# Optimization experiments

Measured on AMD Instinct MI355X. Metric: run time of the kernel, lower is better.

Reference implementation:

```python
import jax, jax.numpy as jnp
import numpy as np

D_MODEL = 1024
D_STATE = 16
DT_RANK = 64  # d_model // 16 ('auto')
DT_MIN = 0.001
DT_MAX = 0.1


def setup_inputs() -> dict:
    key = jax.random.key(0)
    ks = jax.random.split(key, 7)
    B, S = 2, 2048
    return {
        "x": jax.random.normal(ks[0], (B, S, D_MODEL), jnp.float32),
        "w_in": jax.random.normal(ks[1], (D_MODEL, D_MODEL), jnp.float32) / np.sqrt(D_MODEL).astype(np.float32),
        "w_x": jax.random.normal(ks[2], (D_MODEL, DT_RANK + 2 * D_STATE), jnp.float32) / np.sqrt(D_MODEL).astype(np.float32),
        "w_dt": jax.random.normal(ks[3], (DT_RANK, D_MODEL), jnp.float32) / np.sqrt(DT_RANK).astype(np.float32),
        "b_dt": jnp.zeros((D_MODEL,), jnp.float32),
        "A_log": jax.random.normal(ks[5], (D_MODEL, D_STATE), jnp.float32) * 0.5,
        "Dp": jax.random.normal(ks[6], (D_MODEL,), jnp.float32),
    }


def reference(x, w_in, w_x, w_dt, b_dt, A_log, Dp):
    # x: (b, s, d)
    x_in = jnp.einsum('bsd,de->bse', x, w_in)          # in_proj, (b,s,d_inner=d)
    proj = jnp.einsum('bsd,dp->bsp', x_in, w_x)        # x_proj, (b,s,dt_rank+2n)
    dt_low, Bm, Cm = jnp.split(proj, [DT_RANK, DT_RANK + D_STATE], axis=-1)
    # dt_proj + softplus + range scaling -> (b,s,d)
    dt = jax.nn.softplus(jnp.einsum('bsr,rd->bsd', dt_low, w_dt) + b_dt) * (DT_MAX - DT_MIN) + DT_MIN
    A = -jnp.exp(A_log)                                # (d, n), strictly negative

    b, s, d = x.shape
    h0 = jnp.zeros((b, d, D_STATE), x.dtype)

    # time-major streams for scan
    dt_tm = jnp.swapaxes(dt, 0, 1)     # (s,b,d)
    u_tm = jnp.swapaxes(x_in, 0, 1)    # (s,b,d)
    B_tm = jnp.swapaxes(Bm, 0, 1)      # (s,b,n)
    C_tm = jnp.swapaxes(Cm, 0, 1)      # (s,b,n)

    def step(h, inp):
        dtt, ut, bt, ct = inp
        dA = dtt[:, :, None] * A                      # (b,d,n) = dt[b,d]*A[d,n]
        barA = jnp.exp(dA)
        # bar_B = dA; source sums the input term over channel dim d (keepdim)
        inp_term = jnp.einsum('bdn,bn,bd->bn', dA, bt, ut)  # (b,n)
        h = barA * h + inp_term[:, None, :]           # broadcast over d
        y = jnp.einsum('bdn,bn->bd', h, ct) + Dp * ut # (b,d)
        return h, y

    _, ys = jax.lax.scan(step, h0, (dt_tm, u_tm, B_tm, C_tm))  # ys: (s,b,d)
    return jnp.swapaxes(ys, 0, 1)                     # (b,s,d)
```

## Files before the change

kernel.cpp:

```cpp
#include <hip/hip_runtime.h>
#include <hip/hip_bf16.h>

#define D_MODEL 1024
#define D_STATE 16
#define DT_RANK 64
#define SEQ 2048
#define BATCH 2
#define M_TOTAL 4096
#define CHUNKS 64
#define CLEN 32
#define LOG2E 1.44269504088896f

typedef __bf16 bf16x8 __attribute__((ext_vector_type(8)));
typedef float f32x4 __attribute__((ext_vector_type(4)));

__device__ __forceinline__ unsigned short f2bf(float f) {
    union { float f; unsigned int u; } v; v.f = f;
    unsigned int r = v.u + 0x7FFFu + ((v.u >> 16) & 1u);
    return (unsigned short)(r >> 16);
}
__device__ __forceinline__ float bf2f(unsigned short u) {
    union { unsigned int i; float f; } v; v.i = ((unsigned int)u) << 16; return v.f;
}
__device__ __forceinline__ void gload16(const void* g, void* l) {
    __builtin_amdgcn_global_load_lds(
        (const __attribute__((address_space(1))) unsigned int*)g,
        (__attribute__((address_space(3))) unsigned int*)l, 16, 0, 0);
}
__device__ __forceinline__ float fexp2(float x) { return __builtin_amdgcn_exp2f(x); }

__global__ void __launch_bounds__(256) k_setup(const float* __restrict__ x,
                                               const float* __restrict__ win,
                                               const float* __restrict__ wx,
                                               const float* __restrict__ alog,
                                               unsigned short* __restrict__ xb,
                                               unsigned short* __restrict__ wib,
                                               unsigned short* __restrict__ bt,
                                               unsigned short* __restrict__ wxT,
                                               unsigned short* __restrict__ wxBC,
                                               float* __restrict__ aneg,
                                               unsigned short* __restrict__ anegT) {
    __shared__ float tile[32][33];
    int blk = blockIdx.x;
    int t = threadIdx.x;
    if (blk < 4096) {
        int i = blk * 256 + t;
        float4 v = reinterpret_cast<const float4*>(x)[i];
        ushort4 o;
        o.x = f2bf(v.x); o.y = f2bf(v.y); o.z = f2bf(v.z); o.w = f2bf(v.w);
        reinterpret_cast<ushort4*>(xb)[i] = o;
    } else if (blk < 5120) {
        int i = (blk - 4096) * 256 + t;
        float4 v = reinterpret_cast<const float4*>(win)[i];
        ushort4 o;
        o.x = f2bf(v.x); o.y = f2bf(v.y); o.z = f2bf(v.z); o.w = f2bf(v.w);
        reinterpret_cast<ushort4*>(wib)[i] = o;
    } else if (blk < 6144) {
        int blk2 = blk - 5120;
        int bx = blk2 & 31, by = blk2 >> 5;
        int tx = t & 31, ty = t >> 5;
        int xc = bx * 32 + tx;
#pragma unroll
        for (int j = 0; j < 4; j++)
            tile[ty + 8 * j][tx] = win[(by * 32 + ty + 8 * j) * D_MODEL + xc];
        __syncthreads();
        int x2 = by * 32 + tx;
#pragma unroll
        for (int j = 0; j < 4; j++)
            bt[(bx * 32 + ty + 8 * j) * D_MODEL + x2] = f2bf(tile[tx][ty + 8 * j]);
    } else if (blk < 6400) {
        int idx = (blk - 6144) * 256 + t;
        int e = idx & 1023, p = idx >> 10;
        wxT[p * D_MODEL + e] = f2bf(wx[e * 96 + p]);
    } else if (blk < 6528) {
        int idx = (blk - 6400) * 256 + t;
        int e = idx & 1023, p = idx >> 10;
        wxBC[p * D_MODEL + e] = f2bf(wx[e * 96 + 64 + p]);
    } else {
        int i = (blk - 6528) * 256 + t;
        float v = -expf(alog[i]);
        aneg[i] = v * LOG2E;
        anegT[(i & 15) * D_MODEL + (i >> 4)] = f2bf(v);
    }
}

__global__ void __launch_bounds__(256) k_prepgemm(const unsigned short* __restrict__ wxT,
                                                  const unsigned short* __restrict__ wib,
                                                  float* __restrict__ Cp) {
    __shared__ unsigned short sA[2][64 * 32];
    __shared__ unsigned short sB[2][128 * 32];
    int bid = blockIdx.x;
    int n0 = (bid & 7) * 128;
    int ks = bid >> 3;
    int kbase = ks * 128;
    int t = threadIdx.x;
    int lane = t & 63;
    int w = t >> 6;
    int c = lane & 15, q = lane >> 4;

    const unsigned short* ga = wxT + (t >> 2) * D_MODEL + (t & 3) * 8 + kbase;
    const unsigned short* gb = wib + (n0 + (t >> 2)) * D_MODEL + (t & 3) * 8 + kbase;

    f32x4 acc[4][2] = {};
    {
        char* la = (char*)&sA[0][0] + w * 1024;
        char* lb = (char*)&sB[0][0] + w * 1024;
        gload16(ga, la);
        gload16(gb, lb);
        gload16(gb + 64 * D_MODEL, lb + 4096);
    }
    int cur = 0;
    for (int it = 0; it < 4; it++) {
        __syncthreads();
        if (it + 1 < 4) {
            int kn = (it + 1) * 32;
            char* la = (char*)&sA[cur ^ 1][0] + w * 1024;
            char* lb = (char*)&sB[cur ^ 1][0] + w * 1024;
            gload16(ga + kn, la);
            gload16(gb + kn, lb);
            gload16(gb + 64 * D_MODEL + kn, lb + 4096);
        }
        bf16x8 af[4], bfr[2];
#pragma unroll
        for (int i = 0; i < 4; i++)
            af[i] = *reinterpret_cast<const bf16x8*>(&sA[cur][(i * 16 + c) * 32 + q * 8]);
#pragma unroll
        for (int j = 0; j < 2; j++)
            bfr[j] = *reinterpret_cast<const bf16x8*>(&sB[cur][(w * 32 + j * 16 + c) * 32 + q * 8]);
#pragma unroll
        for (int i = 0; i < 4; i++)
#pragma unroll
            for (int j = 0; j < 2; j++)
                acc[i][j] = __builtin_amdgcn_mfma_f32_16x16x32_bf16(bfr[j], af[i], acc[i][j], 0, 0, 0);
        cur ^= 1;
    }
#pragma unroll
    for (int i = 0; i < 4; i++) {
        int p = ks * 64 + i * 16 + c;
#pragma unroll
        for (int j = 0; j < 2; j++) {
            int d = n0 + w * 32 + j * 16 + q * 4;
            *reinterpret_cast<f32x4*>(&Cp[p * D_MODEL + d]) = acc[i][j];
        }
    }
}

__global__ void __launch_bounds__(256) k_prepreduce(const float* __restrict__ Cp,
                                                    float* __restrict__ Tt) {
    int idx = blockIdx.x * 256 + threadIdx.x;
    float s = 0.f;
#pragma unroll
    for (int ks = 0; ks < 8; ks++) s += Cp[ks * 65536 + idx];
    Tt[idx] = s;
}

__global__ void __launch_bounds__(256) k_prep2(const float* __restrict__ wdt,
                                               const float* __restrict__ Tt,
                                               unsigned short* __restrict__ bt) {
    __shared__ float sw[DT_RANK][8];
    int m0 = blockIdx.x * 8;
    int tid = threadIdx.x;
    for (int s = tid; s < DT_RANK * 8; s += 256) {
        int r = s >> 3, rr = s & 7;
        sw[r][rr] = wdt[r * D_MODEL + m0 + rr];
    }
    __syncthreads();
    float acc[8][4] = {};
    for (int r = 0; r < DT_RANK; r++) {
        float tv0 = Tt[r * D_MODEL + tid];
        float tv1 = Tt[r * D_MODEL + tid + 256];
        float tv2 = Tt[r * D_MODEL + tid + 512];
        float tv3 = Tt[r * D_MODEL + tid + 768];
#pragma unroll
        for (int rr = 0; rr < 8; rr++) {
            float wv = sw[r][rr];
            acc[rr][0] = fmaf(wv, tv0, acc[rr][0]);
            acc[rr][1] = fmaf(wv, tv1, acc[rr][1]);
            acc[rr][2] = fmaf(wv, tv2, acc[rr][2]);
            acc[rr][3] = fmaf(wv, tv3, acc[rr][3]);
        }
    }
#pragma unroll
    for (int rr = 0; rr < 8; rr++)
#pragma unroll
        for (int i = 0; i < 4; i++)
            bt[(D_MODEL + m0 + rr) * D_MODEL + tid + i * 256] = f2bf(acc[rr][i]);
}

__global__ void __launch_bounds__(256) k_gemm_big(const unsigned short* __restrict__ xb,
                                                  const unsigned short* __restrict__ bt,
                                                  const float* __restrict__ bdt,
                                                  unsigned short* __restrict__ xinb,
                                                  unsigned short* __restrict__ dtb) {
    __shared__ unsigned short sA[2][128 * 64];
    __shared__ unsigned short sB[2][128 * 64];
    int bid = blockIdx.x;
    int m0 = (bid & 31) * 128;
    int nt = bid >> 5;
    int n0 = nt * 128;
    int t = threadIdx.x;
    int lane = t & 63;
    int w = t >> 6;
    int wm = (w >> 1) * 64, wn = (w & 1) * 64;
    int c = lane & 15, q = lane >> 4;

    const unsigned short* gA[4];
    const unsigned short* gB[4];
#pragma unroll
    for (int L = 0; L < 4; L++) {
        int s = L * 256 + t;
        int row = s >> 3, ch = (s & 7) ^ (row & 7);
        gA[L] = xb + (m0 + row) * D_MODEL + ch * 8;
        gB[L] = bt + (n0 + row) * D_MODEL + ch * 8;
    }

    f32x4 acc[4][4] = {};
    {
        char* la = (char*)&sA[0][0] + w * 1024;
        char* lb = (char*)&sB[0][0] + w * 1024;
#pragma unroll
        for (int L = 0; L < 4; L++) {
            gload16(gA[L], la + L * 4096);
            gload16(gB[L], lb + L * 4096);
        }
    }
    int cur = 0;
    for (int it = 0; it < 16; it++) {
        __syncthreads();
        if (it + 1 < 16) {
            int kn = (it + 1) * 64;
            char* la = (char*)&sA[cur ^ 1][0] + w * 1024;
            char* lb = (char*)&sB[cur ^ 1][0] + w * 1024;
#pragma unroll
            for (int L = 0; L < 4; L++) {
                gload16(gA[L] + kn, la + L * 4096);
                gload16(gB[L] + kn, lb + L * 4096);
            }
        }
#pragma unroll
        for (int kk = 0; kk < 2; kk++) {
            int perm = (((kk << 2) | q) ^ (c & 7)) << 3;
            bf16x8 af[4], bfr[4];
#pragma unroll
            for (int i = 0; i < 4; i++)
                af[i] = *reinterpret_cast<const bf16x8*>(&sA[cur][(wm + i * 16 + c) * 64 + perm]);
#pragma unroll
            for (int j = 0; j < 4; j++)
                bfr[j] = *reinterpret_cast<const bf16x8*>(&sB[cur][(wn + j * 16 + c) * 64 + perm]);
#pragma unroll
            for (int i = 0; i < 4; i++)
#pragma unroll
                for (int j = 0; j < 4; j++)
                    acc[i][j] = __builtin_amdgcn_mfma_f32_16x16x32_bf16(bfr[j], af[i], acc[i][j], 0, 0, 0);
        }
        cur ^= 1;
    }

    if (nt < 8) {
#pragma unroll
        for (int i = 0; i < 4; i++) {
            int row = m0 + wm + i * 16 + c;
#pragma unroll
            for (int j = 0; j < 4; j++) {
                int col = n0 + wn + j * 16 + q * 4;
                ushort4 o;
                o.x = f2bf(acc[i][j][0]); o.y = f2bf(acc[i][j][1]);
                o.z = f2bf(acc[i][j][2]); o.w = f2bf(acc[i][j][3]);
                *reinterpret_cast<ushort4*>(&xinb[row * D_MODEL + col]) = o;
            }
        }
    } else {
#pragma unroll
        for (int i = 0; i < 4; i++) {
            int row = m0 + wm + i * 16 + c;
#pragma unroll
            for (int j = 0; j < 4; j++) {
                int dcol = n0 + wn + j * 16 + q * 4 - D_MODEL;
                float4 bv = *reinterpret_cast<const float4*>(&bdt[dcol]);
                ushort4 o;
                {
                    float xv = acc[i][j][0] + bv.x;
                    float sp = fmaxf(xv, 0.f) + __logf(1.f + __expf(-fabsf(xv)));
                    o.x = f2bf(sp * 0.099f + 0.001f);
                }
                {
                    float xv = acc[i][j][1] + bv.y;
                    float sp = fmaxf(xv, 0.f) + __logf(1.f + __expf(-fabsf(xv)));
                    o.y = f2bf(sp * 0.099f + 0.001f);
                }
                {
                    float xv = acc[i][j][2] + bv.z;
                    float sp = fmaxf(xv, 0.f) + __logf(1.f + __expf(-fabsf(xv)));
                    o.z = f2bf(sp * 0.099f + 0.001f);
                }
                {
                    float xv = acc[i][j][3] + bv.w;
                    float sp = fmaxf(xv, 0.f) + __logf(1.f + __expf(-fabsf(xv)));
                    o.w = f2bf(sp * 0.099f + 0.001f);
                }
                *reinterpret_cast<ushort4*>(&dtb[row * D_MODEL + dcol]) = o;
            }
        }
    }
}

__global__ void __launch_bounds__(256) k_bcw(const unsigned short* __restrict__ xinb,
                                             const unsigned short* __restrict__ dtb,
                                             const unsigned short* __restrict__ wxBC,
                                             const unsigned short* __restrict__ anegT,
                                             float* __restrict__ bcp,
                                             float* __restrict__ wpp) {
    int bid = blockIdx.x;
    int m0 = (bid & 31) * 128;
    int ks = bid >> 5;
    int kbase = ks * 128;
    int t = threadIdx.x;
    int lane = t & 63, w = t >> 6;
    int c = lane & 15, q = lane >> 4;
    int mw = m0 + w * 32;
    f32x4 accb[2][2] = {};
    f32x4 accw[2] = {};
    const unsigned short* pa0 = xinb + (mw + c) * D_MODEL + kbase + q * 8;
    const unsigned short* pa1 = pa0 + 16 * D_MODEL;
    const unsigned short* pt0 = dtb + (mw + c) * D_MODEL + kbase + q * 8;
    const unsigned short* pt1 = pt0 + 16 * D_MODEL;
    const unsigned short* pb0 = wxBC + c * D_MODEL + kbase + q * 8;
    const unsigned short* pb1 = pb0 + 16 * D_MODEL;
    const unsigned short* pA = anegT + c * D_MODEL + kbase + q * 8;
#pragma unroll
    for (int k0 = 0; k0 < 128; k0 += 32) {
        bf16x8 a0 = *reinterpret_cast<const bf16x8*>(pa0 + k0);
        bf16x8 a1 = *reinterpret_cast<const bf16x8*>(pa1 + k0);
        bf16x8 t0 = *reinterpret_cast<const bf16x8*>(pt0 + k0);
        bf16x8 t1 = *reinterpret_cast<const bf16x8*>(pt1 + k0);
        bf16x8 b0 = *reinterpret_cast<const bf16x8*>(pb0 + k0);
        bf16x8 b1 = *reinterpret_cast<const bf16x8*>(pb1 + k0);
        bf16x8 bA = *reinterpret_cast<const bf16x8*>(pA + k0);
        bf16x8 g0, g1;
#pragma unroll
        for (int e = 0; e < 8; e++) {
            g0[e] = (__bf16)((float)t0[e] * (float)a0[e]);
            g1[e] = (__bf16)((float)t1[e] * (float)a1[e]);
        }
        accb[0][0] = __builtin_amdgcn_mfma_f32_16x16x32_bf16(b0, a0, accb[0][0], 0, 0, 0);
        accb[0][1] = __builtin_amdgcn_mfma_f32_16x16x32_bf16(b1, a0, accb[0][1], 0, 0, 0);
        accb[1][0] = __builtin_amdgcn_mfma_f32_16x16x32_bf16(b0, a1, accb[1][0], 0, 0, 0);
        accb[1][1] = __builtin_amdgcn_mfma_f32_16x16x32_bf16(b1, a1, accb[1][1], 0, 0, 0);
        accw[0] = __builtin_amdgcn_mfma_f32_16x16x32_bf16(bA, g0, accw[0], 0, 0, 0);
        accw[1] = __builtin_amdgcn_mfma_f32_16x16x32_bf16(bA, g1, accw[1], 0, 0, 0);
    }
#pragma unroll
    for (int i = 0; i < 2; i++) {
        int row = mw + i * 16 + c;
#pragma unroll
        for (int j = 0; j < 2; j++)
            *reinterpret_cast<f32x4*>(&bcp[(ks * M_TOTAL + row) * 32 + j * 16 + q * 4]) = accb[i][j];
        *reinterpret_cast<f32x4*>(&wpp[(ks * M_TOTAL + row) * 16 + q * 4]) = accw[i];
    }
}

__global__ void __launch_bounds__(256) k_scan1(const unsigned short* __restrict__ dtb,
                                               const float* __restrict__ bcp,
                                               const float* __restrict__ wpp,
                                               const float* __restrict__ aneg,
                                               float* __restrict__ h_loc,
                                               float* __restrict__ dtsum) {
    __shared__ unsigned short s_dt[16][256];
    __shared__ float s_w[16][16];
    int dc = blockIdx.x & 3;
    int c = (blockIdx.x >> 2) & (CHUNKS - 1);
    int b = blockIdx.x >> 8;
    int tid = threadIdx.x;
    int d = dc * 256 + tid;
    float Ad[16];
    const float4* ar = reinterpret_cast<const float4*>(aneg + d * 16);
#pragma unroll
    for (int j = 0; j < 4; j++) {
        float4 a4 = ar[j];
        Ad[4 * j + 0] = a4.x; Ad[4 * j + 1] = a4.y;
        Ad[4 * j + 2] = a4.z; Ad[4 * j + 3] = a4.w;
    }
    float h[16];
#pragma unroll
    for (int n = 0; n < 16; n++) h[n] = 0.f;
    float dts = 0.f;

    int r8 = tid >> 5, col8 = (tid & 31) * 8;
    for (int t0 = 0; t0 < CLEN; t0 += 16) {
        __syncthreads();
        int rowbase = b * SEQ + c * CLEN + t0;
        *reinterpret_cast<uint4*>(&s_dt[r8][col8]) =
            *reinterpret_cast<const uint4*>(dtb + (rowbase + r8) * D_MODEL + dc * 256 + col8);
        *reinterpret_cast<uint4*>(&s_dt[8 + r8][col8]) =
            *reinterpret_cast<const uint4*>(dtb + (rowbase + 8 + r8) * D_MODEL + dc * 256 + col8);
        {
            int r = tid >> 4, n = tid & 15;
            int row = rowbase + r;
            float sB = 0.f, sw = 0.f;
#pragma unroll
            for (int ks = 0; ks < 8; ks++) {
                sB += bcp[(ks * M_TOTAL + row) * 32 + n];
                sw += wpp[(ks * M_TOTAL + row) * 16 + n];
            }
            s_w[r][n] = sB * sw;
        }
        __syncthreads();
        for (int r = 0; r < 16; r++) {
            float dtv = bf2f(s_dt[r][tid]);
            dts += dtv;
#pragma unroll
            for (int n = 0; n < 16; n++) {
                float ba = fexp2(dtv * Ad[n]);
                h[n] = fmaf(ba, h[n], s_w[r][n]);
            }
        }
    }
    int base = ((b * CHUNKS + c) * D_MODEL + d) * 16;
#pragma unroll
    for (int j = 0; j < 4; j++) {
        f32x4 v = {h[4 * j], h[4 * j + 1], h[4 * j + 2], h[4 * j + 3]};
        *reinterpret_cast<f32x4*>(h_loc + base + 4 * j) = v;
    }
    dtsum[(b * CHUNKS + c) * D_MODEL + d] = dts;
}

__global__ void __launch_bounds__(128) k_scan2(float* __restrict__ h_inout,
                                               const float* __restrict__ dtsum,
                                               const float* __restrict__ aneg) {
    int idx = blockIdx.x * 128 + threadIdx.x;
    int n = idx & 15;
    int d = (idx >> 4) & (D_MODEL - 1);
    int b = idx >> 14;
    float A = aneg[d * 16 + n];
    float H = 0.f;
    int off0 = b * CHUNKS * D_MODEL + d;
#pragma unroll 1
    for (int g = 0; g < CHUNKS; g += 8) {
        float hl[8], ds[8];
#pragma unroll
        for (int j = 0; j < 8; j++) {
            int off = off0 + (g + j) * D_MODEL;
            hl[j] = h_inout[off * 16 + n];
            ds[j] = dtsum[off];
        }
#pragma unroll
        for (int j = 0; j < 8; j++) {
            int off = off0 + (g + j) * D_MODEL;
            float P = fexp2(ds[j] * A);
            h_inout[off * 16 + n] = H;
            H = fmaf(P, H, hl[j]);
        }
    }
}

__global__ void __launch_bounds__(256) k_scan3(const unsigned short* __restrict__ dtb,
                                               const unsigned short* __restrict__ xinb,
                                               const float* __restrict__ bcp,
                                               const float* __restrict__ wpp,
                                               const float* __restrict__ aneg,
                                               const float* __restrict__ dp,
                                               const float* __restrict__ H_in,
                                               float* __restrict__ out) {
    __shared__ unsigned short s_dt[16][256], s_u[16][256];
    __shared__ float s_w[16][16], s_c[16][16];
    int dc = blockIdx.x & 3;
    int c = (blockIdx.x >> 2) & (CHUNKS - 1);
    int b = blockIdx.x >> 8;
    int tid = threadIdx.x;
    int d = dc * 256 + tid;
    float Ad[16];
    const float4* ar = reinterpret_cast<const float4*>(aneg + d * 16);
#pragma unroll
    for (int j = 0; j < 4; j++) {
        float4 a4 = ar[j];
        Ad[4 * j + 0] = a4.x; Ad[4 * j + 1] = a4.y;
        Ad[4 * j + 2] = a4.z; Ad[4 * j + 3] = a4.w;
    }
    float Dpd = dp[d];
    float h[16];
    int base = ((b * CHUNKS + c) * D_MODEL + d) * 16;
#pragma unroll
    for (int j = 0; j < 4; j++) {
        f32x4 v = *reinterpret_cast<const f32x4*>(H_in + base + 4 * j);
        h[4 * j] = v[0]; h[4 * j + 1] = v[1]; h[4 * j + 2] = v[2]; h[4 * j + 3] = v[3];
    }

    int r8 = tid >> 5, col8 = (tid & 31) * 8;
    for (int t0 = 0; t0 < CLEN; t0 += 16) {
        __syncthreads();
        int rowbase = b * SEQ + c * CLEN + t0;
        *reinterpret_cast<uint4*>(&s_dt[r8][col8]) =
            *reinterpret_cast<const uint4*>(dtb + (rowbase + r8) * D_MODEL + dc * 256 + col8);
        *reinterpret_cast<uint4*>(&s_dt[8 + r8][col8]) =
            *reinterpret_cast<const uint4*>(dtb + (rowbase + 8 + r8) * D_MODEL + dc * 256 + col8);
        *reinterpret_cast<uint4*>(&s_u[r8][col8]) =
            *reinterpret_cast<const uint4*>(xinb + (rowbase + r8) * D_MODEL + dc * 256 + col8);
        *reinterpret_cast<uint4*>(&s_u[8 + r8][col8]) =
            *reinterpret_cast<const uint4*>(xinb + (rowbase + 8 + r8) * D_MODEL + dc * 256 + col8);
        {
            int r = tid >> 4, n = tid & 15;
            int row = rowbase + r;
            float sB = 0.f, sw = 0.f, sC = 0.f;
#pragma unroll
            for (int ks = 0; ks < 8; ks++) {
                sB += bcp[(ks * M_TOTAL + row) * 32 + n];
                sC += bcp[(ks * M_TOTAL + row) * 32 + 16 + n];
                sw += wpp[(ks * M_TOTAL + row) * 16 + n];
            }
            s_w[r][n] = sB * sw;
            s_c[r][n] = sC;
        }
        __syncthreads();
        for (int r = 0; r < 16; r++) {
            float dtv = bf2f(s_dt[r][tid]), uv = bf2f(s_u[r][tid]);
            float y = Dpd * uv;
#pragma unroll
            for (int n = 0; n < 16; n++) {
                float ba = fexp2(dtv * Ad[n]);
                h[n] = fmaf(ba, h[n], s_w[r][n]);
                y = fmaf(h[n], s_c[r][n], y);
            }
            out[(rowbase + r) * D_MODEL + d] = y;
        }
    }
}

extern "C" void kernel_launch(void* const* d_in, const int* in_sizes, int n_in,
                              void* d_out, int out_size, void* d_ws, size_t ws_size,
                              hipStream_t stream) {
    const float* x     = (const float*)d_in[0];
    const float* w_in  = (const float*)d_in[1];
    const float* w_x   = (const float*)d_in[2];
    const float* w_dt  = (const float*)d_in[3];
    const float* b_dt  = (const float*)d_in[4];
    const float* A_log = (const float*)d_in[5];
    const float* Dp    = (const float*)d_in[6];
    float* out = (float*)d_out;

    char* ws = (char*)d_ws;
    unsigned short* xb   = (unsigned short*)(ws + 0);
    unsigned short* bt   = (unsigned short*)(ws + 8388608);
    float* Tt            = (float*)(ws + 12845056);
    float* aneg          = (float*)(ws + 13107200);
    unsigned short* xinb = (unsigned short*)(ws + 13959168);
    unsigned short* dtb  = (unsigned short*)(ws + 22347776);
    unsigned short* wib  = (unsigned short*)(ws + 22347776);
    unsigned short* wxT  = (unsigned short*)(ws + 24444928);
    float* Cp            = (float*)(ws + 24707072);
    unsigned short* wxBC = (unsigned short*)(ws + 30736384);
    float* bcp           = (float*)(ws + 30801920);
    float* wpp           = (float*)(ws + 34996224);
    unsigned short* anegT= (unsigned short*)(ws + 37093376);
    float* h_loc         = (float*)(ws + 0);
    float* dtsum         = (float*)(ws + 8388608);

    k_setup<<<6592, 256, 0, stream>>>(x, w_in, w_x, A_log, xb, wib, bt, wxT, wxBC, aneg, anegT);
    k_prepgemm<<<64, 256, 0, stream>>>(wxT, wib, Cp);
    k_prepreduce<<<256, 256, 0, stream>>>(Cp, Tt);
    k_prep2<<<128, 256, 0, stream>>>(w_dt, Tt, bt);
    k_gemm_big<<<512, 256, 0, stream>>>(xb, bt, b_dt, xinb, dtb);
    k_bcw<<<256, 256, 0, stream>>>(xinb, dtb, wxBC, anegT, bcp, wpp);
    k_scan1<<<BATCH * CHUNKS * 4, 256, 0, stream>>>(dtb, bcp, wpp, aneg, h_loc, dtsum);
    k_scan2<<<256, 128, 0, stream>>>(h_loc, dtsum, aneg);
    k_scan3<<<BATCH * CHUNKS * 4, 256, 0, stream>>>(dtb, xinb, bcp, wpp, aneg, Dp, h_loc, out);
}
```

Measured before the change: 175.7 us.

## Unfold precomputed dt weight product into in_proj GEMM plus low-rank GEMMs

Drops the weight-folding prep (w_in·w_x·w_dt), which doubled the N dimension of the main GEMM. The path is now an N=1024 in_proj GEMM, then a split-K GEMM producing the 64-wide dt_low from x_in, then a K=64 GEMM with fused softplus that produces dt. This roughly halves the main GEMM's FLOPs and removes three prep kernels. In exchange it adds a partial-sum buffer and its reduction, plus one more dependent launch. Numerics also shift slightly because dt is now computed from bf16-rounded x_in.

```diff
diff --git a/kernel.cpp b/kernel.cpp
--- a/kernel.cpp
+++ b/kernel.cpp
@@ -32,12 +32,13 @@
 __global__ void __launch_bounds__(256) k_setup(const float* __restrict__ x,
                                                const float* __restrict__ win,
                                                const float* __restrict__ wx,
+                                               const float* __restrict__ wdt,
                                                const float* __restrict__ alog,
                                                unsigned short* __restrict__ xb,
-                                               unsigned short* __restrict__ wib,
                                                unsigned short* __restrict__ bt,
                                                unsigned short* __restrict__ wxT,
                                                unsigned short* __restrict__ wxBC,
+                                               unsigned short* __restrict__ wdtT,
                                                float* __restrict__ aneg,
                                                unsigned short* __restrict__ anegT) {
     __shared__ float tile[32][33];
@@ -50,13 +51,7 @@
         o.x = f2bf(v.x); o.y = f2bf(v.y); o.z = f2bf(v.z); o.w = f2bf(v.w);
         reinterpret_cast<ushort4*>(xb)[i] = o;
     } else if (blk < 5120) {
-        int i = (blk - 4096) * 256 + t;
-        float4 v = reinterpret_cast<const float4*>(win)[i];
-        ushort4 o;
-        o.x = f2bf(v.x); o.y = f2bf(v.y); o.z = f2bf(v.z); o.w = f2bf(v.w);
-        reinterpret_cast<ushort4*>(wib)[i] = o;
-    } else if (blk < 6144) {
-        int blk2 = blk - 5120;
+        int blk2 = blk - 4096;
         int bx = blk2 & 31, by = blk2 >> 5;
         int tx = t & 31, ty = t >> 5;
         int xc = bx * 32 + tx;
@@ -68,161 +63,63 @@
 #pragma unroll
         for (int j = 0; j < 4; j++)
             bt[(bx * 32 + ty + 8 * j) * D_MODEL + x2] = f2bf(tile[tx][ty + 8 * j]);
-    } else if (blk < 6400) {
-        int idx = (blk - 6144) * 256 + t;
+    } else if (blk < 5376) {
+        int idx = (blk - 5120) * 256 + t;
         int e = idx & 1023, p = idx >> 10;
         wxT[p * D_MODEL + e] = f2bf(wx[e * 96 + p]);
-    } else if (blk < 6528) {
-        int idx = (blk - 6400) * 256 + t;
+    } else if (blk < 5504) {
+        int idx = (blk - 5376) * 256 + t;
         int e = idx & 1023, p = idx >> 10;
         wxBC[p * D_MODEL + e] = f2bf(wx[e * 96 + 64 + p]);
-    } else {
-        int i = (blk - 6528) * 256 + t;
+    } else if (blk < 5568) {
+        int i = (blk - 5504) * 256 + t;
         float v = -expf(alog[i]);
         aneg[i] = v * LOG2E;
         anegT[(i & 15) * D_MODEL + (i >> 4)] = f2bf(v);
-    }
-}
-
-__global__ void __launch_bounds__(256) k_prepgemm(const unsigned short* __restrict__ wxT,
-                                                  const unsigned short* __restrict__ wib,
-                                                  float* __restrict__ Cp) {
-    __shared__ unsigned short sA[2][64 * 32];
-    __shared__ unsigned short sB[2][128 * 32];
+    } else {
+        int idx = (blk - 5568) * 256 + t;
+        int d = idx & 1023, k = idx >> 10;
+        wdtT[d * DT_RANK + k] = f2bf(wdt[k * D_MODEL + d]);
+    }
+}
+
+__global__ void __launch_bounds__(256) k_gemm_xin(const unsigned short* __restrict__ xb,
+                                                  const unsigned short* __restrict__ bt,
+                                                  unsigned short* __restrict__ xinb) {
+    __shared__ unsigned short sA[2][64 * 64];
+    __shared__ unsigned short sB[2][128 * 64];
     int bid = blockIdx.x;
-    int n0 = (bid & 7) * 128;
-    int ks = bid >> 3;
-    int kbase = ks * 128;
+    int m0 = (bid & 63) * 64;
+    int n0 = (bid >> 6) * 128;
     int t = threadIdx.x;
     int lane = t & 63;
     int w = t >> 6;
+    int wm = (w >> 1) * 32, wn = (w & 1) * 64;
     int c = lane & 15, q = lane >> 4;
 
-    const unsigned short* ga = wxT + (t >> 2) * D_MODEL + (t & 3) * 8 + kbase;
-    const unsigned short* gb = wib + (n0 + (t >> 2)) * D_MODEL + (t & 3) * 8 + kbase;
-
-    f32x4 acc[4][2] = {};
+    const unsigned short* gA[2];
+    const unsigned short* gB[4];
+#pragma unroll
+    for (int L = 0; L < 2; L++) {
+        int s = L * 256 + t;
+        int row = s >> 3, ch = (s & 7) ^ (row & 7);
+        gA[L] = xb + (m0 + row) * D_MODEL + ch * 8;
+    }
+#pragma unroll
+    for (int L = 0; L < 4; L++) {
+        int s = L * 256 + t;
+        int row = s >> 3, ch = (s & 7) ^ (row & 7);
+        gB[L] = bt + (n0 + row) * D_MODEL + ch * 8;
+    }
+
+    f32x4 acc[2][4] = {};
     {
         char* la = (char*)&sA[0][0] + w * 1024;
         char* lb = (char*)&sB[0][0] + w * 1024;
-        gload16(ga, la);
-        gload16(gb, lb);
-        gload16(gb + 64 * D_MODEL, lb + 4096);
-    }
-    int cur = 0;
-    for (int it = 0; it < 4; it++) {
-        __syncthreads();
-        if (it + 1 < 4) {
-            int kn = (it + 1) * 32;
-            char* la = (char*)&sA[cur ^ 1][0] + w * 1024;
-            char* lb = (char*)&sB[cur ^ 1][0] + w * 1024;
-            gload16(ga + kn, la);
-            gload16(gb + kn, lb);
-            gload16(gb + 64 * D_MODEL + kn, lb + 4096);
-        }
-        bf16x8 af[4], bfr[2];
-#pragma unroll
-        for (int i = 0; i < 4; i++)
-            af[i] = *reinterpret_cast<const bf16x8*>(&sA[cur][(i * 16 + c) * 32 + q * 8]);
-#pragma unroll
-        for (int j = 0; j < 2; j++)
-            bfr[j] = *reinterpret_cast<const bf16x8*>(&sB[cur][(w * 32 + j * 16 + c) * 32 + q * 8]);
-#pragma unroll
-        for (int i = 0; i < 4; i++)
-#pragma unroll
-            for (int j = 0; j < 2; j++)
-                acc[i][j] = __builtin_amdgcn_mfma_f32_16x16x32_bf16(bfr[j], af[i], acc[i][j], 0, 0, 0);
-        cur ^= 1;
-    }
-#pragma unroll
-    for (int i = 0; i < 4; i++) {
-        int p = ks * 64 + i * 16 + c;
-#pragma unroll
-        for (int j = 0; j < 2; j++) {
-            int d = n0 + w * 32 + j * 16 + q * 4;
-            *reinterpret_cast<f32x4*>(&Cp[p * D_MODEL + d]) = acc[i][j];
-        }
-    }
-}
-
-__global__ void __launch_bounds__(256) k_prepreduce(const float* __restrict__ Cp,
-                                                    float* __restrict__ Tt) {
-    int idx = blockIdx.x * 256 + threadIdx.x;
-    float s = 0.f;
-#pragma unroll
-    for (int ks = 0; ks < 8; ks++) s += Cp[ks * 65536 + idx];
-    Tt[idx] = s;
-}
-
-__global__ void __launch_bounds__(256) k_prep2(const float* __restrict__ wdt,
-                                               const float* __restrict__ Tt,
-                                               unsigned short* __restrict__ bt) {
-    __shared__ float sw[DT_RANK][8];
-    int m0 = blockIdx.x * 8;
-    int tid = threadIdx.x;
-    for (int s = tid; s < DT_RANK * 8; s += 256) {
-        int r = s >> 3, rr = s & 7;
-        sw[r][rr] = wdt[r * D_MODEL + m0 + rr];
-    }
-    __syncthreads();
-    float acc[8][4] = {};
-    for (int r = 0; r < DT_RANK; r++) {
-        float tv0 = Tt[r * D_MODEL + tid];
-        float tv1 = Tt[r * D_MODEL + tid + 256];
-        float tv2 = Tt[r * D_MODEL + tid + 512];
-        float tv3 = Tt[r * D_MODEL + tid + 768];
-#pragma unroll
-        for (int rr = 0; rr < 8; rr++) {
-            float wv = sw[r][rr];
-            acc[rr][0] = fmaf(wv, tv0, acc[rr][0]);
-            acc[rr][1] = fmaf(wv, tv1, acc[rr][1]);
-            acc[rr][2] = fmaf(wv, tv2, acc[rr][2]);
-            acc[rr][3] = fmaf(wv, tv3, acc[rr][3]);
-        }
-    }
-#pragma unroll
-    for (int rr = 0; rr < 8; rr++)
-#pragma unroll
-        for (int i = 0; i < 4; i++)
-            bt[(D_MODEL + m0 + rr) * D_MODEL + tid + i * 256] = f2bf(acc[rr][i]);
-}
-
-__global__ void __launch_bounds__(256) k_gemm_big(const unsigned short* __restrict__ xb,
-                                                  const unsigned short* __restrict__ bt,
-                                                  const float* __restrict__ bdt,
-                                                  unsigned short* __restrict__ xinb,
-                                                  unsigned short* __restrict__ dtb) {
-    __shared__ unsigned short sA[2][128 * 64];
-    __shared__ unsigned short sB[2][128 * 64];
-    int bid = blockIdx.x;
-    int m0 = (bid & 31) * 128;
-    int nt = bid >> 5;
-    int n0 = nt * 128;
-    int t = threadIdx.x;
-    int lane = t & 63;
-    int w = t >> 6;
-    int wm = (w >> 1) * 64, wn = (w & 1) * 64;
-    int c = lane & 15, q = lane >> 4;
-
-    const unsigned short* gA[4];
-    const unsigned short* gB[4];
-#pragma unroll
-    for (int L = 0; L < 4; L++) {
-        int s = L * 256 + t;
-        int row = s >> 3, ch = (s & 7) ^ (row & 7);
-        gA[L] = xb + (m0 + row) * D_MODEL + ch * 8;
-        gB[L] = bt + (n0 + row) * D_MODEL + ch * 8;
-    }
-
-    f32x4 acc[4][4] = {};
-    {
-        char* la = (char*)&sA[0][0] + w * 1024;
-        char* lb = (char*)&sB[0][0] + w * 1024;
-#pragma unroll
-        for (int L = 0; L < 4; L++) {
-            gload16(gA[L], la + L * 4096);
-            gload16(gB[L], lb + L * 4096);
-        }
+#pragma unroll
+        for (int L = 0; L < 2; L++) gload16(gA[L], la + L * 4096);
+#pragma unroll
+        for (int L = 0; L < 4; L++) gload16(gB[L], lb + L * 4096);
     }
     int cur = 0;
     for (int it = 0; it < 16; it++) {
@@ -232,74 +129,159 @@
             char* la = (char*)&sA[cur ^ 1][0] + w * 1024;
             char* lb = (char*)&sB[cur ^ 1][0] + w * 1024;
 #pragma unroll
-            for (int L = 0; L < 4; L++) {
-                gload16(gA[L] + kn, la + L * 4096);
-                gload16(gB[L] + kn, lb + L * 4096);
-            }
+            for (int L = 0; L < 2; L++) gload16(gA[L] + kn, la + L * 4096);
+#pragma unroll
+            for (int L = 0; L < 4; L++) gload16(gB[L] + kn, lb + L * 4096);
         }
 #pragma unroll
         for (int kk = 0; kk < 2; kk++) {
             int perm = (((kk << 2) | q) ^ (c & 7)) << 3;
-            bf16x8 af[4], bfr[4];
-#pragma unroll
-            for (int i = 0; i < 4; i++)
+            bf16x8 af[2], bfr[4];
+#pragma unroll
+            for (int i = 0; i < 2; i++)
                 af[i] = *reinterpret_cast<const bf16x8*>(&sA[cur][(wm + i * 16 + c) * 64 + perm]);
 #pragma unroll
             for (int j = 0; j < 4; j++)
                 bfr[j] = *reinterpret_cast<const bf16x8*>(&sB[cur][(wn + j * 16 + c) * 64 + perm]);
 #pragma unroll
-            for (int i = 0; i < 4; i++)
+            for (int i = 0; i < 2; i++)
 #pragma unroll
                 for (int j = 0; j < 4; j++)
                     acc[i][j] = __builtin_amdgcn_mfma_f32_16x16x32_bf16(bfr[j], af[i], acc[i][j], 0, 0, 0);
         }
         cur ^= 1;
     }
-
-    if (nt < 8) {
-#pragma unroll
-        for (int i = 0; i < 4; i++) {
-            int row = m0 + wm + i * 16 + c;
-#pragma unroll
-            for (int j = 0; j < 4; j++) {
-                int col = n0 + wn + j * 16 + q * 4;
-                ushort4 o;
-                o.x = f2bf(acc[i][j][0]); o.y = f2bf(acc[i][j][1]);
-                o.z = f2bf(acc[i][j][2]); o.w = f2bf(acc[i][j][3]);
-                *reinterpret_cast<ushort4*>(&xinb[row * D_MODEL + col]) = o;
-            }
-        }
-    } else {
-#pragma unroll
-        for (int i = 0; i < 4; i++) {
-            int row = m0 + wm + i * 16 + c;
-#pragma unroll
-            for (int j = 0; j < 4; j++) {
-                int dcol = n0 + wn + j * 16 + q * 4 - D_MODEL;
-                float4 bv = *reinterpret_cast<const float4*>(&bdt[dcol]);
-                ushort4 o;
-                {
-                    float xv = acc[i][j][0] + bv.x;
-                    float sp = fmaxf(xv, 0.f) + __logf(1.f + __expf(-fabsf(xv)));
-                    o.x = f2bf(sp * 0.099f + 0.001f);
-                }
-                {
-                    float xv = acc[i][j][1] + bv.y;
-                    float sp = fmaxf(xv, 0.f) + __logf(1.f + __expf(-fabsf(xv)));
-                    o.y = f2bf(sp * 0.099f + 0.001f);
-                }
-                {
-                    float xv = acc[i][j][2] + bv.z;
-                    float sp = fmaxf(xv, 0.f) + __logf(1.f + __expf(-fabsf(xv)));
-                    o.z = f2bf(sp * 0.099f + 0.001f);
-                }
-                {
-                    float xv = acc[i][j][3] + bv.w;
-                    float sp = fmaxf(xv, 0.f) + __logf(1.f + __expf(-fabsf(xv)));
-                    o.w = f2bf(sp * 0.099f + 0.001f);
-                }
-                *reinterpret_cast<ushort4*>(&dtb[row * D_MODEL + dcol]) = o;
-            }
+#pragma unroll
+    for (int i = 0; i < 2; i++) {
+        int row = m0 + wm + i * 16 + c;
+#pragma unroll
+        for (int j = 0; j < 4; j++) {
+            int col = n0 + wn + j * 16 + q * 4;
+            ushort4 o;
+            o.x = f2bf(acc[i][j][0]); o.y = f2bf(acc[i][j][1]);
+            o.z = f2bf(acc[i][j][2]); o.w = f2bf(acc[i][j][3]);
+            *reinterpret_cast<ushort4*>(&xinb[row * D_MODEL + col]) = o;
+        }
+    }
+}
+
+__global__ void __launch_bounds__(256) k_xlow(const unsigned short* __restrict__ xinb,
+                                              const unsigned short* __restrict__ wxT,
+                                              float* __restrict__ xlp) {
+    int bid = blockIdx.x;
+    int m0 = (bid & 31) * 128;
+    int ks = bid >> 5;
+    int kbase = ks * 128;
+    int t = threadIdx.x;
+    int lane = t & 63, w = t >> 6;
+    int c = lane & 15, q = lane >> 4;
+    int mw = m0 + w * 32;
+    f32x4 acc[2][4] = {};
+    const unsigned short* pa0 = xinb + (mw + c) * D_MODEL + kbase + q * 8;
+    const unsigned short* pa1 = pa0 + 16 * D_MODEL;
+    const unsigned short* pw = wxT + c * D_MODEL + kbase + q * 8;
+#pragma unroll
+    for (int k0 = 0; k0 < 128; k0 += 32) {
+        bf16x8 a0 = *reinterpret_cast<const bf16x8*>(pa0 + k0);
+        bf16x8 a1 = *reinterpret_cast<const bf16x8*>(pa1 + k0);
+#pragma unroll
+        for (int j = 0; j < 4; j++) {
+            bf16x8 wf = *reinterpret_cast<const bf16x8*>(pw + j * 16 * D_MODEL + k0);
+            acc[0][j] = __builtin_amdgcn_mfma_f32_16x16x32_bf16(wf, a0, acc[0][j], 0, 0, 0);
+            acc[1][j] = __builtin_amdgcn_mfma_f32_16x16x32_bf16(wf, a1, acc[1][j], 0, 0, 0);
+        }
+    }
+#pragma unroll
+    for (int i = 0; i < 2; i++) {
+        int row = mw + i * 16 + c;
+#pragma unroll
+        for (int j = 0; j < 4; j++)
+            *reinterpret_cast<f32x4*>(&xlp[(ks * M_TOTAL + row) * DT_RANK + j * 16 + q * 4]) = acc[i][j];
+    }
+}
+
+__global__ void __launch_bounds__(256) k_gemm_dt(const float* __restrict__ xlp,
+                                                 const unsigned short* __restrict__ wdtT,
+                                                 const float* __restrict__ bdt,
+                                                 unsigned short* __restrict__ dtb) {
+    __shared__ unsigned short sA[128 * 64];
+    int bid = blockIdx.x;
+    int m0 = (bid & 31) * 128;
+    int n0 = (bid >> 5) * 128;
+    int t = threadIdx.x;
+    int lane = t & 63, w = t >> 6;
+    int c = lane & 15, q = lane >> 4;
+
+    {
+        int row = t >> 1, half = t & 1;
+        int gbase = (m0 + row) * DT_RANK;
+#pragma unroll
+        for (int ch = 0; ch < 4; ch++) {
+            int col8 = half * 4 + ch;
+            f32x4 s0 = {}, s1 = {};
+#pragma unroll
+            for (int ksi = 0; ksi < 8; ksi++) {
+                const f32x4* p = reinterpret_cast<const f32x4*>(
+                    xlp + ksi * (M_TOTAL * DT_RANK) + gbase + col8 * 8);
+                s0 += p[0];
+                s1 += p[1];
+            }
+            int swz = col8 ^ (row & 7);
+            ushort4 lo, hi;
+            lo.x = f2bf(s0[0]); lo.y = f2bf(s0[1]); lo.z = f2bf(s0[2]); lo.w = f2bf(s0[3]);
+            hi.x = f2bf(s1[0]); hi.y = f2bf(s1[1]); hi.z = f2bf(s1[2]); hi.w = f2bf(s1[3]);
+            *reinterpret_cast<ushort4*>(&sA[row * 64 + swz * 8]) = lo;
+            *reinterpret_cast<ushort4*>(&sA[row * 64 + swz * 8 + 4]) = hi;
+        }
+    }
+    __syncthreads();
+
+    int mw = m0 + w * 32;
+    f32x4 acc[2][8] = {};
+#pragma unroll
+    for (int kk = 0; kk < 2; kk++) {
+        bf16x8 af[2];
+#pragma unroll
+        for (int i = 0; i < 2; i++)
+            af[i] = *reinterpret_cast<const bf16x8*>(
+                &sA[(w * 32 + i * 16 + c) * 64 + ((((kk << 2) | q)) ^ (c & 7)) * 8]);
+#pragma unroll
+        for (int j = 0; j < 8; j++) {
+            bf16x8 bfr = *reinterpret_cast<const bf16x8*>(
+                &wdtT[(n0 + j * 16 + c) * DT_RANK + kk * 32 + q * 8]);
+            acc[0][j] = __builtin_amdgcn_mfma_f32_16x16x32_bf16(bfr, af[0], acc[0][j], 0, 0, 0);
+            acc[1][j] = __builtin_amdgcn_mfma_f32_16x16x32_bf16(bfr, af[1], acc[1][j], 0, 0, 0);
+        }
+    }
+#pragma unroll
+    for (int i = 0; i < 2; i++) {
+        int row = mw + i * 16 + c;
+#pragma unroll
+        for (int j = 0; j < 8; j++) {
+            int dcol = n0 + j * 16 + q * 4;
+            float4 bv = *reinterpret_cast<const float4*>(&bdt[dcol]);
+            ushort4 o;
+            {
+                float xv = acc[i][j][0] + bv.x;
+                float sp = fmaxf(xv, 0.f) + __logf(1.f + __expf(-fabsf(xv)));
+                o.x = f2bf(sp * 0.099f + 0.001f);
+            }
+            {
+                float xv = acc[i][j][1] + bv.y;
+                float sp = fmaxf(xv, 0.f) + __logf(1.f + __expf(-fabsf(xv)));
+                o.y = f2bf(sp * 0.099f + 0.001f);
+            }
+            {
+                float xv = acc[i][j][2] + bv.z;
+                float sp = fmaxf(xv, 0.f) + __logf(1.f + __expf(-fabsf(xv)));
+                o.z = f2bf(sp * 0.099f + 0.001f);
+            }
+            {
+                float xv = acc[i][j][3] + bv.w;
+                float sp = fmaxf(xv, 0.f) + __logf(1.f + __expf(-fabsf(xv)));
+                o.w = f2bf(sp * 0.099f + 0.001f);
+            }
+            *reinterpret_cast<ushort4*>(&dtb[row * D_MODEL + dcol]) = o;
         }
     }
 }
@@ -540,25 +522,23 @@
     char* ws = (char*)d_ws;
     unsigned short* xb   = (unsigned short*)(ws + 0);
     unsigned short* bt   = (unsigned short*)(ws + 8388608);
-    float* Tt            = (float*)(ws + 12845056);
-    float* aneg          = (float*)(ws + 13107200);
-    unsigned short* xinb = (unsigned short*)(ws + 13959168);
-    unsigned short* dtb  = (unsigned short*)(ws + 22347776);
-    unsigned short* wib  = (unsigned short*)(ws + 22347776);
-    unsigned short* wxT  = (unsigned short*)(ws + 24444928);
-    float* Cp            = (float*)(ws + 24707072);
-    unsigned short* wxBC = (unsigned short*)(ws + 30736384);
-    float* bcp           = (float*)(ws + 30801920);
-    float* wpp           = (float*)(ws + 34996224);
-    unsigned short* anegT= (unsigned short*)(ws + 37093376);
+    unsigned short* xinb = (unsigned short*)(ws + 10485760);
+    unsigned short* dtb  = (unsigned short*)(ws + 18874368);
+    float* xlp           = (float*)(ws + 27262976);
+    float* bcp           = (float*)(ws + 27262976);
+    float* wpp           = (float*)(ws + 31457280);
+    unsigned short* wxT  = (unsigned short*)(ws + 35651584);
+    unsigned short* wxBC = (unsigned short*)(ws + 35782656);
+    unsigned short* wdtT = (unsigned short*)(ws + 35848192);
+    float* aneg          = (float*)(ws + 35979264);
+    unsigned short* anegT= (unsigned short*)(ws + 36044800);
     float* h_loc         = (float*)(ws + 0);
     float* dtsum         = (float*)(ws + 8388608);
 
-    k_setup<<<6592, 256, 0, stream>>>(x, w_in, w_x, A_log, xb, wib, bt, wxT, wxBC, aneg, anegT);
-    k_prepgemm<<<64, 256, 0, stream>>>(wxT, wib, Cp);
-    k_prepreduce<<<256, 256, 0, stream>>>(Cp, Tt);
-    k_prep2<<<128, 256, 0, stream>>>(w_dt, Tt, bt);
-    k_gemm_big<<<512, 256, 0, stream>>>(xb, bt, b_dt, xinb, dtb);
+    k_setup<<<5824, 256, 0, stream>>>(x, w_in, w_x, w_dt, A_log, xb, bt, wxT, wxBC, wdtT, aneg, anegT);
+    k_gemm_xin<<<512, 256, 0, stream>>>(xb, bt, xinb);
+    k_xlow<<<256, 256, 0, stream>>>(xinb, wxT, xlp);
+    k_gemm_dt<<<256, 256, 0, stream>>>(xlp, wdtT, b_dt, dtb);
     k_bcw<<<256, 256, 0, stream>>>(xinb, dtb, wxBC, anegT, bcp, wpp);
     k_scan1<<<BATCH * CHUNKS * 4, 256, 0, stream>>>(dtb, bcp, wpp, aneg, h_loc, dtsum);
     k_scan2<<<256, 128, 0, stream>>>(h_loc, dtsum, aneg);
```

Result: no change. 175.4 us (-0.2%).
